# Kernel optimization log

Measured on AMD Instinct MI355X. Metric: run time of the kernel, lower is better.

Reference implementation:

```python
import jax, jax.numpy as jnp
import numpy as np

T, B, D, H, F, E = 2048, 2, 1024, 16, 4096, 8
HD = D // H
EPS = 1.1920929e-07  # torch.finfo(float32).eps


def setup_inputs() -> dict:
    key = jax.random.key(0)
    ks = jax.random.split(key, 20)
    sc = D ** -0.5
    n = lambda k, shape, s: jax.random.normal(k, shape, jnp.float32) * s
    return {
        "x": jax.random.normal(ks[0], (T, B, D), jnp.float32),
        "Wq": n(ks[1], (D, D), sc), "bq": jnp.zeros((D,), jnp.float32),
        "Wk": n(ks[2], (D, D), sc), "bk": jnp.zeros((D,), jnp.float32),
        "Wv": n(ks[3], (D, D), sc), "bv": jnp.zeros((D,), jnp.float32),
        "Wo": n(ks[4], (D, D), sc), "bo": jnp.zeros((D,), jnp.float32),
        "ln1_g": jnp.ones((D,), jnp.float32), "ln1_b": jnp.zeros((D,), jnp.float32),
        "ln2_g": jnp.ones((D,), jnp.float32), "ln2_b": jnp.zeros((D,), jnp.float32),
        "wg": n(ks[5], (D, E), sc),
        "W1": n(ks[6], (E, D, F), sc), "b1": jnp.zeros((E, F), jnp.float32),
        "W2": n(ks[7], (E, F, D), F ** -0.5), "b2": jnp.zeros((E, D), jnp.float32),
    }


def layer_norm(x, g, b):
    m = jnp.mean(x, -1, keepdims=True)
    v = jnp.var(x, -1, keepdims=True)
    return (x - m) * jax.lax.rsqrt(v + 1e-5) * g + b


def attention(x, Wq, bq, Wk, bk, Wv, bv, Wo, bo):
    t, b, d = x.shape
    q = ((x @ Wq + bq) * (HD ** -0.5)).reshape(t, b, H, HD)
    k = (x @ Wk + bk).reshape(t, b, H, HD)
    v = (x @ Wv + bv).reshape(t, b, H, HD)
    a = jax.nn.softmax(jnp.einsum('tbhd,sbhd->bhts', q, k), axis=-1)
    o = jnp.einsum('bhts,sbhd->tbhd', a, v).reshape(t, b, d)
    return o @ Wo + bo


def moe(xf, wg, W1, b1, W2, b2):
    # xf: [S, D] tokens (batch-major order, matching x.transpose(0,1).reshape(-1,d))
    S = xf.shape[0]
    C = 2 * ((S + E - 1) // E)  # fairseq top2 train capacity
    logits = xf.astype(jnp.float32) @ wg.astype(jnp.float32)
    gates = jax.nn.softmax(logits, axis=-1)
    idx1 = jnp.argmax(gates, axis=-1)
    m1 = jax.nn.one_hot(idx1, E, dtype=jnp.int32)
    idx2 = jnp.argmax(jnp.where(m1 > 0, -jnp.inf, logits), axis=-1)
    m2 = jax.nn.one_hot(idx2, E, dtype=jnp.int32)
    g1 = jnp.take_along_axis(gates, idx1[:, None], 1)[:, 0]
    g2 = jnp.take_along_axis(gates, idx2[:, None], 1)[:, 0]
    loc1 = jnp.cumsum(m1, axis=0) - 1
    loc2 = jnp.cumsum(m2, axis=0) - 1 + jnp.sum(m1, axis=0, keepdims=True)
    pos1 = jnp.sum(loc1 * m1, axis=1)
    pos2 = jnp.sum(loc2 * m2, axis=1)
    l_aux = jnp.mean(jnp.mean(gates, 0) * jnp.mean(m1.astype(jnp.float32), 0)) * E * E
    k1 = (pos1 < C).astype(xf.dtype)
    k2 = (pos2 < C).astype(xf.dtype)
    g1 = g1.astype(xf.dtype) * k1
    g2 = g2.astype(xf.dtype) * k2
    den = jnp.maximum(g1 + g2, EPS)
    g1, g2 = g1 / den, g2 / den
    f1 = idx1 * C + jnp.minimum(pos1, C - 1)
    f2 = idx2 * C + jnp.minimum(pos2, C - 1)
    # dispatch (unweighted, capacity-masked)
    buf = jnp.zeros((E * C, D), xf.dtype)
    buf = buf.at[f1].add(xf * k1[:, None]).at[f2].add(xf * k2[:, None])
    h = jax.nn.relu(jnp.einsum('ecd,edf->ecf', buf.reshape(E, C, D), W1) + b1[:, None, :])
    out = (jnp.einsum('ecf,efd->ecd', h, W2) + b2[:, None, :]).reshape(E * C, D)
    # combine with normalized gates (dropped tokens have zero gate)
    y = g1[:, None] * out[f1] + g2[:, None] * out[f2]
    return y, l_aux


def reference(x, Wq, bq, Wk, bk, Wv, bv, Wo, bo, ln1_g, ln1_b, ln2_g, ln2_b, wg, W1, b1, W2, b2):
    # pre-LN self-attention block
    residual = x
    h = layer_norm(x, ln1_g, ln1_b)
    h = attention(h, Wq, bq, Wk, bk, Wv, bv, Wo, bo)
    x = residual + h
    # pre-LN MoE FFN block
    residual = x
    h = layer_norm(x, ln2_g, ln2_b)
    hb = jnp.swapaxes(h, 0, 1).reshape(-1, D)  # [B*T, D]
    y, l_aux = moe(hb, wg, W1, b1, W2, b2)
    y = jnp.swapaxes(y.reshape(B, T, D), 0, 1)
    x = residual + y
    return x, l_aux
```

## Files before the change

kernel.cpp:

```cpp
#include <hip/hip_runtime.h>

#define TT 2048
#define BB 2
#define DD 1024
#define HH 16
#define HD 64
#define FF 4096
#define EE 8
#define SS (TT*BB)
#define CAP 1024
#define EPSF 1.1920929e-07f

typedef __attribute__((ext_vector_type(8))) short short8;
typedef __attribute__((ext_vector_type(4))) float floatx4;

static __device__ inline unsigned short f2bf(float f){
    unsigned int u = __float_as_uint(f);
    unsigned int r = (u + 0x7fffu + ((u>>16)&1u)) >> 16;
    return (unsigned short)r;
}
static __device__ inline float bf2f(unsigned short h){
    return __uint_as_float(((unsigned int)h)<<16);
}
static __device__ inline void split2(float x, unsigned short& h, unsigned short& l){
    unsigned short hh = f2bf(x);
    h = hh;
    l = f2bf(x - bf2f(hh));
}
#define GETF4(v,j) ((j)==0?(v).x:(j)==1?(v).y:(j)==2?(v).z:(v).w)

__global__ __launch_bounds__(256) void ln_kernel(const float* __restrict__ x,
    const float* __restrict__ gam, const float* __restrict__ bet, float* __restrict__ o)
{
    int row = blockIdx.x;
    int tid = threadIdx.x;
    float4 v = ((const float4*)(x + (size_t)row*DD))[tid];
    float s  = v.x+v.y+v.z+v.w;
    float ss = v.x*v.x+v.y*v.y+v.z*v.z+v.w*v.w;
    __shared__ float r1[256], r2[256];
    r1[tid]=s; r2[tid]=ss;
    __syncthreads();
    for (int off=128; off>0; off>>=1){
        if (tid<off){ r1[tid]+=r1[tid+off]; r2[tid]+=r2[tid+off]; }
        __syncthreads();
    }
    float mean = r1[0] * (1.f/DD);
    float var  = r2[0] * (1.f/DD) - mean*mean;
    float inv  = 1.f / sqrtf(var + 1e-5f);
    float4 g = ((const float4*)gam)[tid];
    float4 b = ((const float4*)bet)[tid];
    float4 r;
    r.x = (v.x-mean)*inv*g.x + b.x;
    r.y = (v.y-mean)*inv*g.y + b.y;
    r.z = (v.z-mean)*inv*g.z + b.z;
    r.w = (v.w-mean)*inv*g.w + b.w;
    ((float4*)(o + (size_t)row*DD))[tid] = r;
}

__global__ __launch_bounds__(256) void ln_split_kernel(const float* __restrict__ x,
    const float* __restrict__ gam, const float* __restrict__ bet,
    unsigned short* __restrict__ oh, unsigned short* __restrict__ ol)
{
    int row = blockIdx.x;
    int tid = threadIdx.x;
    float4 v = ((const float4*)(x + (size_t)row*DD))[tid];
    float s  = v.x+v.y+v.z+v.w;
    float ss = v.x*v.x+v.y*v.y+v.z*v.z+v.w*v.w;
    __shared__ float r1[256], r2[256];
    r1[tid]=s; r2[tid]=ss;
    __syncthreads();
    for (int off=128; off>0; off>>=1){
        if (tid<off){ r1[tid]+=r1[tid+off]; r2[tid]+=r2[tid+off]; }
        __syncthreads();
    }
    float mean = r1[0] * (1.f/DD);
    float var  = r2[0] * (1.f/DD) - mean*mean;
    float inv  = 1.f / sqrtf(var + 1e-5f);
    float4 g = ((const float4*)gam)[tid];
    float4 b = ((const float4*)bet)[tid];
    float4 r;
    r.x = (v.x-mean)*inv*g.x + b.x;
    r.y = (v.y-mean)*inv*g.y + b.y;
    r.z = (v.z-mean)*inv*g.z + b.z;
    r.w = (v.w-mean)*inv*g.w + b.w;
    ushort4 hv, lv;
    split2(r.x, hv.x, lv.x);
    split2(r.y, hv.y, lv.y);
    split2(r.z, hv.z, lv.z);
    split2(r.w, hv.w, lv.w);
    ((ushort4*)(oh + (size_t)row*DD))[tid] = hv;
    ((ushort4*)(ol + (size_t)row*DD))[tid] = lv;
}

template<bool RELU, bool OUTBF16>
__global__ __launch_bounds__(256) void gemm_mfma(
    const unsigned short* __restrict__ A, const unsigned short* __restrict__ Bt,
    const float* __restrict__ bias, float* __restrict__ Cf,
    unsigned short* __restrict__ Cb,
    int M, int N, int K, long wStride, int bStride, int rowsPerExp)
{
    __shared__ unsigned short As[128*64];
    __shared__ unsigned short Bs[128*64];
    const int tid = threadIdx.x, lane = tid&63;
    const int w = tid>>6, wr = w>>1, wc = w&1;
    int gx = gridDim.x;
    int nwg = gx*gridDim.y;
    int flat = blockIdx.y*gx + blockIdx.x;
    int qq = nwg>>3;
    flat = (flat&7)*qq + (flat>>3);
    const int m0 = (flat/gx)*128, n0 = (flat%gx)*128;
    const int e = m0 / rowsPerExp;
    const unsigned short* Bp = Bt + (size_t)e*wStride;
    const int srow = tid>>3, sslot = tid&7;
    floatx4 zf = {0.f,0.f,0.f,0.f};
    floatx4 acc[4][4];
    #pragma unroll
    for (int m=0;m<4;m++)
        #pragma unroll
        for (int n=0;n<4;n++) acc[m][n]=zf;

    short8 ar[4], br[4];
    #pragma unroll
    for (int i=0;i<4;i++){
        int r = srow + i*32;
        ar[i] = *(const short8*)(A  + (size_t)(m0+r)*K + sslot*8);
        br[i] = *(const short8*)(Bp + (size_t)(n0+r)*K + sslot*8);
    }
    const int NT = K/64;
    for (int kt=0; kt<NT; kt++){
        __syncthreads();
        #pragma unroll
        for (int i=0;i<4;i++){
            int r = srow + i*32;
            int off = r*64 + ((sslot ^ (r&7))<<3);
            *(short8*)(&As[off]) = ar[i];
            *(short8*)(&Bs[off]) = br[i];
        }
        __syncthreads();
        if (kt+1 < NT){
            int k0 = (kt+1)*64;
            #pragma unroll
            for (int i=0;i<4;i++){
                int r = srow + i*32;
                ar[i] = *(const short8*)(A  + (size_t)(m0+r)*K + k0 + sslot*8);
                br[i] = *(const short8*)(Bp + (size_t)(n0+r)*K + k0 + sslot*8);
            }
        }
        #pragma unroll
        for (int kk=0;kk<2;kk++){
            short8 af[4], bf[4];
            int kgrp = kk*4 + (lane>>4);
            #pragma unroll
            for (int m=0;m<4;m++){
                int rowa = wr*64 + m*16 + (lane&15);
                af[m] = *(const short8*)(&As[rowa*64 + ((kgrp ^ (rowa&7))<<3)]);
                int rowb = wc*64 + m*16 + (lane&15);
                bf[m] = *(const short8*)(&Bs[rowb*64 + ((kgrp ^ (rowb&7))<<3)]);
            }
            #pragma unroll
            for (int m=0;m<4;m++)
                #pragma unroll
                for (int n=0;n<4;n++)
                    acc[m][n] = __builtin_amdgcn_mfma_f32_16x16x32_bf16(af[m], bf[n], acc[m][n], 0,0,0);
        }
    }
    int colg = n0 + wc*64 + (lane&15);
    int rowg = m0 + wr*64 + ((lane>>4)<<2);
    #pragma unroll
    for (int n=0;n<4;n++){
        float bv = bias[e*bStride + colg + n*16];
        #pragma unroll
        for (int m=0;m<4;m++){
            #pragma unroll
            for (int i2=0;i2<4;i2++){
                float v = acc[m][n][i2] + bv;
                if (RELU) v = fmaxf(v, 0.f);
                size_t o = (size_t)(rowg + m*16 + i2)*N + colg + n*16;
                if (OUTBF16) Cb[o] = f2bf(v); else Cf[o] = v;
            }
        }
    }
}

template<bool QKV>
__global__ __launch_bounds__(256) void gemm_mfma_s(
    const unsigned short* __restrict__ Ahi, const unsigned short* __restrict__ Alo,
    const unsigned short* __restrict__ Bhi, const unsigned short* __restrict__ Blo,
    const float* __restrict__ b0, const float* __restrict__ b1p, const float* __restrict__ b2p,
    const float* __restrict__ res,
    float* __restrict__ o0,
    unsigned short* __restrict__ kh, unsigned short* __restrict__ kl,
    unsigned short* __restrict__ vh,
    int M, int K)
{
    __shared__ unsigned short As[128*64];
    __shared__ unsigned short Bs[128*64];
    const int tid = threadIdx.x, lane = tid&63;
    const int w = tid>>6, wr = w>>1, wc = w&1;
    const int m0 = blockIdx.y*128, n0 = blockIdx.x*128;
    const int row = tid>>1, khalf = tid&1;
    floatx4 zf = {0.f,0.f,0.f,0.f};
    floatx4 acc[4][4];
    #pragma unroll
    for (int m=0;m<4;m++)
        #pragma unroll
        for (int n=0;n<4;n++) acc[m][n]=zf;

    short8 awh0,awh1,awl0,awl1, bwh0,bwh1,bwl0,bwl1;
    {
        size_t ao = (size_t)(m0+row)*K + khalf*16;
        awh0 = *(const short8*)(Ahi+ao); awh1 = *(const short8*)(Ahi+ao+8);
        awl0 = *(const short8*)(Alo+ao); awl1 = *(const short8*)(Alo+ao+8);
        size_t bo = (size_t)(n0+row)*K + khalf*16;
        bwh0 = *(const short8*)(Bhi+bo); bwh1 = *(const short8*)(Bhi+bo+8);
        bwl0 = *(const short8*)(Blo+bo); bwl1 = *(const short8*)(Blo+bo+8);
    }
    const int NT = K/32;
    for (int kt=0; kt<NT; kt++){
        __syncthreads();
        {
            int base = row*64, sw = row&7;
            int g0 = khalf*2, g1 = khalf*2+1;
            *(short8*)(&As[base + ((g0^sw)<<3)])     = awh0;
            *(short8*)(&As[base + ((g1^sw)<<3)])     = awh1;
            *(short8*)(&As[base + (((g0+4)^sw)<<3)]) = awl0;
            *(short8*)(&As[base + (((g1+4)^sw)<<3)]) = awl1;
            *(short8*)(&Bs[base + ((g0^sw)<<3)])     = bwh0;
            *(short8*)(&Bs[base + ((g1^sw)<<3)])     = bwh1;
            *(short8*)(&Bs[base + (((g0+4)^sw)<<3)]) = bwl0;
            *(short8*)(&Bs[base + (((g1+4)^sw)<<3)]) = bwl1;
        }
        __syncthreads();
        if (kt+1 < NT){
            int k0 = (kt+1)*32;
            size_t ao = (size_t)(m0+row)*K + k0 + khalf*16;
            awh0 = *(const short8*)(Ahi+ao); awh1 = *(const short8*)(Ahi+ao+8);
            awl0 = *(const short8*)(Alo+ao); awl1 = *(const short8*)(Alo+ao+8);
            size_t bo = (size_t)(n0+row)*K + k0 + khalf*16;
            bwh0 = *(const short8*)(Bhi+bo); bwh1 = *(const short8*)(Bhi+bo+8);
            bwl0 = *(const short8*)(Blo+bo); bwl1 = *(const short8*)(Blo+bo+8);
        }
        {
            int kg = lane>>4;
            short8 afh[4], afl[4], bfh[4], bfl[4];
            #pragma unroll
            for (int m=0;m<4;m++){
                int ra = wr*64 + m*16 + (lane&15);
                afh[m] = *(const short8*)(&As[ra*64 + ((kg ^ (ra&7))<<3)]);
                afl[m] = *(const short8*)(&As[ra*64 + (((kg+4) ^ (ra&7))<<3)]);
                int rb = wc*64 + m*16 + (lane&15);
                bfh[m] = *(const short8*)(&Bs[rb*64 + ((kg ^ (rb&7))<<3)]);
                bfl[m] = *(const short8*)(&Bs[rb*64 + (((kg+4) ^ (rb&7))<<3)]);
            }
            #pragma unroll
            for (int m=0;m<4;m++)
                #pragma unroll
                for (int n=0;n<4;n++){
                    acc[m][n] = __builtin_amdgcn_mfma_f32_16x16x32_bf16(afl[m], bfh[n], acc[m][n], 0,0,0);
                    acc[m][n] = __builtin_amdgcn_mfma_f32_16x16x32_bf16(afh[m], bfl[n], acc[m][n], 0,0,0);
                    acc[m][n] = __builtin_amdgcn_mfma_f32_16x16x32_bf16(afh[m], bfh[n], acc[m][n], 0,0,0);
                }
        }
    }
    int colg = n0 + wc*64 + (lane&15);
    int rowg = m0 + wr*64 + ((lane>>4)<<2);
    if (QKV){
        int chunk = n0>>10;
        int colc = colg & 1023;
        const float* bp = chunk==0 ? b0 : (chunk==1 ? b1p : b2p);
        #pragma unroll
        for (int n=0;n<4;n++){
            float bv = bp[colc + n*16];
            #pragma unroll
            for (int m=0;m<4;m++){
                #pragma unroll
                for (int i2=0;i2<4;i2++){
                    int r = rowg + m*16 + i2;
                    float v = acc[m][n][i2] + bv;
                    size_t off = (size_t)r*DD + colc + n*16;
                    if (chunk==0){
                        o0[off] = v*0.125f;
                    } else if (chunk==1){
                        unsigned short hh, ll;
                        split2(v, hh, ll);
                        kh[off]=hh; kl[off]=ll;
                    } else {
                        vh[off] = f2bf(v);
                    }
                }
            }
        }
    } else {
        #pragma unroll
        for (int n=0;n<4;n++){
            float bv = b0[colg + n*16];
            #pragma unroll
            for (int m=0;m<4;m++){
                #pragma unroll
                for (int i2=0;i2<4;i2++){
                    int r = rowg + m*16 + i2;
                    float v = acc[m][n][i2] + bv + res[(size_t)r*DD + colg + n*16];
                    o0[(size_t)r*DD + colg + n*16] = v;
                }
            }
        }
    }
}

__global__ __launch_bounds__(512) void attn_mfma(const float* __restrict__ q,
    const unsigned short* __restrict__ khi, const unsigned short* __restrict__ klo,
    const unsigned short* __restrict__ vbf,
    unsigned short* __restrict__ ohi, unsigned short* __restrict__ olo)
{
    __shared__ unsigned short Kh[128*64], Kl[128*64];
    __shared__ unsigned short Vb[64*128];
    __shared__ unsigned short Ph[8*16*64];
    const int tid = threadIdx.x, lane = tid&63, w = tid>>6;
    const int t0 = blockIdx.x*128;
    const int b = blockIdx.y>>4, h = blockIdx.y&15;

    short8 qh[2], ql[2];
    #pragma unroll
    for (int kk=0;kk<2;kk++){
        const float* qp = q + ((size_t)(t0 + 16*w + (lane&15))*BB + b)*DD + h*64 + kk*32 + (lane>>4)*8;
        float4 f0 = ((const float4*)qp)[0];
        float4 f1 = ((const float4*)qp)[1];
        unsigned short hh[8], ll[8];
        #pragma unroll
        for (int j=0;j<4;j++){ split2(GETF4(f0,j), hh[j], ll[j]); }
        #pragma unroll
        for (int j=0;j<4;j++){ split2(GETF4(f1,j), hh[4+j], ll[4+j]); }
        qh[kk] = *(short8*)hh; ql[kk] = *(short8*)ll;
    }

    const int kr = tid>>2, kq = tid&3;
    const int vs0 = (tid&63)*2, vd0 = (tid>>6)*8;
    short8 kwh0,kwh1,kwl0,kwl1, vw0,vw1;
    {
        size_t ko = ((size_t)kr*BB + b)*DD + h*64 + kq*16;
        kwh0 = *(const short8*)(khi+ko); kwh1 = *(const short8*)(khi+ko+8);
        kwl0 = *(const short8*)(klo+ko); kwl1 = *(const short8*)(klo+ko+8);
        size_t vo = ((size_t)vs0*BB + b)*DD + h*64 + vd0;
        vw0 = *(const short8*)(vbf+vo);
        vw1 = *(const short8*)(vbf+vo + (size_t)BB*DD);
    }

    float m_st[4] = {-3.0e38f,-3.0e38f,-3.0e38f,-3.0e38f};
    float l_st[4] = {0.f,0.f,0.f,0.f};
    floatx4 zf = {0.f,0.f,0.f,0.f};
    floatx4 oacc[4];
    #pragma unroll
    for (int n=0;n<4;n++) oacc[n]=zf;

    for (int s0=0; s0<TT; s0+=128){
        __syncthreads();
        {
            int base = kr*64, sw = kr&7;
            int g0 = kq*2, g1 = kq*2+1;
            *(short8*)(&Kh[base + ((g0^sw)<<3)]) = kwh0;
            *(short8*)(&Kh[base + ((g1^sw)<<3)]) = kwh1;
            *(short8*)(&Kl[base + ((g0^sw)<<3)]) = kwl0;
            *(short8*)(&Kl[base + ((g1^sw)<<3)]) = kwl1;
        }
        {
            int g = vs0>>3, so = vs0&7;
            #pragma unroll
            for (int j=0;j<8;j++){
                int d = vd0 + j;
                ushort2 pv;
                pv.x = (unsigned short)vw0[j];
                pv.y = (unsigned short)vw1[j];
                *(ushort2*)(&Vb[d*128 + ((g ^ (d&7))<<3) + so]) = pv;
            }
        }
        __syncthreads();
        if (s0+128 < TT){
            size_t ko = ((size_t)(s0+128+kr)*BB + b)*DD + h*64 + kq*16;
            kwh0 = *(const short8*)(khi+ko); kwh1 = *(const short8*)(khi+ko+8);
            kwl0 = *(const short8*)(klo+ko); kwl1 = *(const short8*)(klo+ko+8);
            size_t vo = ((size_t)(s0+128+vs0)*BB + b)*DD + h*64 + vd0;
            vw0 = *(const short8*)(vbf+vo);
            vw1 = *(const short8*)(vbf+vo + (size_t)BB*DD);
        }
        floatx4 sacc[8];
        __builtin_amdgcn_s_setprio(1);
        #pragma unroll
        for (int n=0;n<8;n++){
            floatx4 s = zf;
            #pragma unroll
            for (int kk=0;kk<2;kk++){
                int g = kk*4 + (lane>>4);
                int rb = n*16 + (lane&15);
                short8 kbh = *(const short8*)(&Kh[rb*64 + ((g ^ (rb&7))<<3)]);
                short8 kbl = *(const short8*)(&Kl[rb*64 + ((g ^ (rb&7))<<3)]);
                s = __builtin_amdgcn_mfma_f32_16x16x32_bf16(ql[kk], kbh, s, 0,0,0);
                s = __builtin_amdgcn_mfma_f32_16x16x32_bf16(qh[kk], kbl, s, 0,0,0);
                s = __builtin_amdgcn_mfma_f32_16x16x32_bf16(qh[kk], kbh, s, 0,0,0);
            }
            sacc[n] = s;
        }
        __builtin_amdgcn_s_setprio(0);
        float mx[4];
        #pragma unroll
        for (int r=0;r<4;r++){
            float a0 = fmaxf(fmaxf(sacc[0][r], sacc[1][r]), fmaxf(sacc[2][r], sacc[3][r]));
            float a1 = fmaxf(fmaxf(sacc[4][r], sacc[5][r]), fmaxf(sacc[6][r], sacc[7][r]));
            mx[r] = fmaxf(a0, a1);
        }
        #pragma unroll
        for (int sh=1; sh<16; sh<<=1){
            #pragma unroll
            for (int r=0;r<4;r++) mx[r] = fmaxf(mx[r], __shfl_xor(mx[r], sh));
        }
        float corr[4];
        #pragma unroll
        for (int r=0;r<4;r++){
            float nm = fmaxf(m_st[r], mx[r]);
            corr[r] = __expf(m_st[r] - nm);
            m_st[r] = nm;
        }
        float ts[4] = {0.f,0.f,0.f,0.f};
        #pragma unroll
        for (int n=0;n<8;n++){
            #pragma unroll
            for (int r=0;r<4;r++){
                float p = __expf(sacc[n][r] - m_st[r]);
                ts[r] += p;
                sacc[n][r] = p;
            }
        }
        #pragma unroll
        for (int sh=1; sh<16; sh<<=1){
            #pragma unroll
            for (int r=0;r<4;r++) ts[r] += __shfl_xor(ts[r], sh);
        }
        #pragma unroll
        for (int r=0;r<4;r++) l_st[r] = l_st[r]*corr[r] + ts[r];
        #pragma unroll
        for (int n=0;n<4;n++)
            #pragma unroll
            for (int r=0;r<4;r++) oacc[n][r] *= corr[r];
        #pragma unroll
        for (int half=0; half<2; half++){
            #pragma unroll
            for (int n2=0;n2<4;n2++){
                int n = half*4 + n2;
                #pragma unroll
                for (int r=0;r<4;r++){
                    int q2 = ((lane>>4)<<2) + r;
                    int s2 = n2*16 + (lane&15);
                    int off = w*1024 + q2*64 + (((s2>>3) ^ (q2&7))<<3) + (s2&7);
                    Ph[off] = f2bf(sacc[n][r]);
                }
            }
            __builtin_amdgcn_s_setprio(1);
            #pragma unroll
            for (int kk=0;kk<2;kk++){
                int g = kk*4 + (lane>>4);
                int rq = lane&15;
                short8 pa = *(const short8*)(&Ph[w*1024 + rq*64 + ((g ^ (rq&7))<<3)]);
                #pragma unroll
                for (int n=0;n<4;n++){
                    int rd = n*16 + (lane&15);
                    int gv = half*8 + g;
                    short8 vb = *(const short8*)(&Vb[rd*128 + ((gv ^ (rd&7))<<3)]);
                    oacc[n] = __builtin_amdgcn_mfma_f32_16x16x32_bf16(pa, vb, oacc[n], 0,0,0);
                }
            }
            __builtin_amdgcn_s_setprio(0);
        }
    }
    float il[4];
    #pragma unroll
    for (int r=0;r<4;r++) il[r] = 1.f/l_st[r];
    int qrow = t0 + 16*w + ((lane>>4)<<2);
    #pragma unroll
    for (int n=0;n<4;n++){
        #pragma unroll
        for (int r=0;r<4;r++){
            float v = oacc[n][r]*il[r];
            unsigned short hh, ll;
            split2(v, hh, ll);
            size_t off = ((size_t)(qrow+r)*BB + b)*DD + h*64 + n*16 + (lane&15);
            ohi[off] = hh; olo[off] = ll;
        }
    }
}

__global__ __launch_bounds__(256) void transpose_bf16_k(const float* __restrict__ in,
    unsigned short* __restrict__ outp, int R, int C)
{
    __shared__ float t[64][65];
    int e = blockIdx.z;
    const float* ip = in + (size_t)e*R*C;
    unsigned short* op = outp + (size_t)e*R*C;
    int r0 = blockIdx.y*64, c0 = blockIdx.x*64;
    int tid = threadIdx.x;
    #pragma unroll
    for (int i=0;i<4;i++){
        int ch = i*256 + tid;
        int r = ch>>4, c4 = (ch&15)*4;
        float4 v = *(const float4*)(ip + (size_t)(r0+r)*C + c0 + c4);
        t[r][c4+0]=v.x; t[r][c4+1]=v.y; t[r][c4+2]=v.z; t[r][c4+3]=v.w;
    }
    __syncthreads();
    #pragma unroll
    for (int i=0;i<4;i++){
        int ch = i*256 + tid;
        int rr = ch>>4, c4 = (ch&15)*4;
        ushort4 o;
        o.x = f2bf(t[c4+0][rr]); o.y = f2bf(t[c4+1][rr]);
        o.z = f2bf(t[c4+2][rr]); o.w = f2bf(t[c4+3][rr]);
        *(ushort4*)(op + (size_t)(c0+rr)*R + r0 + c4) = o;
    }
}

__global__ __launch_bounds__(256) void transpose_split_k(const float* __restrict__ in,
    unsigned short* __restrict__ oh, unsigned short* __restrict__ ol, int R, int C)
{
    __shared__ float t[64][65];
    int r0 = blockIdx.y*64, c0 = blockIdx.x*64;
    int tid = threadIdx.x;
    #pragma unroll
    for (int i=0;i<4;i++){
        int ch = i*256 + tid;
        int r = ch>>4, c4 = (ch&15)*4;
        float4 v = *(const float4*)(in + (size_t)(r0+r)*C + c0 + c4);
        t[r][c4+0]=v.x; t[r][c4+1]=v.y; t[r][c4+2]=v.z; t[r][c4+3]=v.w;
    }
    __syncthreads();
    #pragma unroll
    for (int i=0;i<4;i++){
        int ch = i*256 + tid;
        int rr = ch>>4, c4 = (ch&15)*4;
        ushort4 hv, lv;
        split2(t[c4+0][rr], hv.x, lv.x);
        split2(t[c4+1][rr], hv.y, lv.y);
        split2(t[c4+2][rr], hv.z, lv.z);
        split2(t[c4+3][rr], hv.w, lv.w);
        size_t off = (size_t)(c0+rr)*R + r0 + c4;
        *(ushort4*)(oh + off) = hv;
        *(ushort4*)(ol + off) = lv;
    }
}

__global__ __launch_bounds__(256) void gather_bf16_k(const float* __restrict__ h2,
    const int* __restrict__ s2r, unsigned short* __restrict__ buf)
{
    int s = blockIdx.x; int row = s2r[s]; int c = threadIdx.x;
    float4 v = make_float4(0.f,0.f,0.f,0.f);
    if (row>=0) v = *(const float4*)(h2 + (size_t)row*DD + c*4);
    ushort4 o;
    o.x=f2bf(v.x); o.y=f2bf(v.y); o.z=f2bf(v.z); o.w=f2bf(v.w);
    *(ushort4*)(buf + (size_t)s*DD + c*4) = o;
}

__global__ __launch_bounds__(256) void route_kernel(const float* __restrict__ h2,
    const float* __restrict__ wgm, float* __restrict__ gates,
    int* __restrict__ idx1, int* __restrict__ idx2,
    float* __restrict__ g1, float* __restrict__ g2)
{
    int wid = threadIdx.x >> 6, lane = threadIdx.x & 63;
    int s = blockIdx.x*4 + wid;
    int row = (s % TT)*BB + (s / TT);
    const float* hr = h2 + (size_t)row*DD;
    float acc[EE] = {};
    #pragma unroll
    for (int c=0;c<16;c++){
        int d = c*64 + lane;
        float xv = hr[d];
        const float* wr = wgm + (size_t)d*EE;
        #pragma unroll
        for (int e2=0;e2<EE;e2++) acc[e2] += xv * wr[e2];
    }
    #pragma unroll
    for (int off=32; off>0; off>>=1){
        #pragma unroll
        for (int e2=0;e2<EE;e2++) acc[e2] += __shfl_down(acc[e2], off);
    }
    if (lane==0){
        float mx = acc[0];
        #pragma unroll
        for (int e2=1;e2<EE;e2++) mx = fmaxf(mx, acc[e2]);
        float ex[EE]; float sum=0.f;
        #pragma unroll
        for (int e2=0;e2<EE;e2++){ ex[e2] = __expf(acc[e2]-mx); sum += ex[e2]; }
        float inv = 1.f/sum;
        int i1=0; float bv1=acc[0];
        #pragma unroll
        for (int e2=1;e2<EE;e2++){ if (acc[e2] > bv1){ bv1=acc[e2]; i1=e2; } }
        int i2=-1; float bv2=-3.0e38f;
        #pragma unroll
        for (int e2=0;e2<EE;e2++){ if (e2!=i1 && acc[e2] > bv2){ bv2=acc[e2]; i2=e2; } }
        #pragma unroll
        for (int e2=0;e2<EE;e2++) gates[(size_t)s*EE + e2] = ex[e2]*inv;
        idx1[s]=i1; idx2[s]=i2;
        g1[s]=ex[i1]*inv; g2[s]=ex[i2]*inv;
    }
}

__global__ __launch_bounds__(256) void scan_kernel(
    const float* __restrict__ gates, const int* __restrict__ idx1, const int* __restrict__ idx2,
    const float* __restrict__ g1, const float* __restrict__ g2,
    float* __restrict__ g1n, float* __restrict__ g2n,
    int* __restrict__ f1, int* __restrict__ f2, int* __restrict__ slot2row,
    float* __restrict__ laux)
{
    __shared__ int i1s[SS];
    __shared__ int i2s[SS];
    __shared__ int cnt1[256][EE];
    __shared__ int cnt2[256][EE];
    __shared__ float gsum[256][EE];
    __shared__ int tot1[EE];
    int tid = threadIdx.x;
    for (int i=tid;i<EE*CAP;i+=256) slot2row[i] = -1;
    for (int i=tid;i<SS;i+=256){ i1s[i]=idx1[i]; i2s[i]=idx2[i]; }
    __syncthreads();
    int c1l[EE]={}, c2l[EE]={};
    float gl[EE]={};
    int base = tid*16;
    for (int qq=0;qq<16;qq++){
        int s = base+qq;
        c1l[i1s[s]]++; c2l[i2s[s]]++;
        #pragma unroll
        for (int e2=0;e2<EE;e2++) gl[e2] += gates[(size_t)s*EE+e2];
    }
    #pragma unroll
    for (int e2=0;e2<EE;e2++){ cnt1[tid][e2]=c1l[e2]; cnt2[tid][e2]=c2l[e2]; gsum[tid][e2]=gl[e2]; }
    __syncthreads();
    if (tid < EE){
        int e2 = tid;
        int run=0;
        for (int t=0;t<256;t++){ int tmp=cnt1[t][e2]; cnt1[t][e2]=run; run+=tmp; }
        tot1[e2]=run;
        run=0;
        for (int t=0;t<256;t++){ int tmp=cnt2[t][e2]; cnt2[t][e2]=run; run+=tmp; }
        float gr=0.f;
        for (int t=0;t<256;t++) gr += gsum[t][e2];
        gsum[0][e2]=gr;
    }
    __syncthreads();
    int p1[EE], p2[EE];
    #pragma unroll
    for (int e2=0;e2<EE;e2++){ p1[e2]=cnt1[tid][e2]; p2[e2]=cnt2[tid][e2]+tot1[e2]; }
    for (int qq=0;qq<16;qq++){
        int s = base+qq;
        int e1 = i1s[s], e2v = i2s[s];
        int pos1 = p1[e1]++;
        int pos2 = p2[e2v]++;
        float gv1 = g1[s], gv2 = g2[s];
        float gm1 = (pos1<CAP)? gv1 : 0.f;
        float gm2 = (pos2<CAP)? gv2 : 0.f;
        float den = fmaxf(gm1+gm2, EPSF);
        g1n[s] = gm1/den; g2n[s] = gm2/den;
        int ff1 = e1*CAP + (pos1<CAP?pos1:CAP-1);
        int ff2 = e2v*CAP + (pos2<CAP?pos2:CAP-1);
        f1[s]=ff1; f2[s]=ff2;
        int hrow = (s % TT)*BB + (s / TT);
        if (pos1<CAP) slot2row[ff1]=hrow;
        if (pos2<CAP) slot2row[ff2]=hrow;
    }
    if (tid==0){
        float a=0.f;
        #pragma unroll
        for (int e2=0;e2<EE;e2++) a += (gsum[0][e2]*(1.f/SS)) * ((float)tot1[e2]*(1.f/SS));
        laux[0] = a * (float)EE;
    }
}

__global__ __launch_bounds__(256) void combine_kernel(const float* __restrict__ x2,
    const float* __restrict__ eout, const float* __restrict__ g1n, const float* __restrict__ g2n,
    const int* __restrict__ f1, const int* __restrict__ f2, float* __restrict__ out)
{
    int s = blockIdx.x;
    float a = g1n[s], b = g2n[s];
    int s1 = f1[s], s2 = f2[s];
    int row = (s % TT)*BB + (s / TT);
    int c = threadIdx.x;
    float4 o1 = ((const float4*)(eout + (size_t)s1*DD))[c];
    float4 o2 = ((const float4*)(eout + (size_t)s2*DD))[c];
    float4 xr = ((const float4*)(x2 + (size_t)row*DD))[c];
    float4 r;
    r.x = xr.x + a*o1.x + b*o2.x;
    r.y = xr.y + a*o1.y + b*o2.y;
    r.z = xr.z + a*o1.z + b*o2.z;
    r.w = xr.w + a*o1.w + b*o2.w;
    ((float4*)(out + (size_t)row*DD))[c] = r;
}

extern "C" void kernel_launch(void* const* d_in, const int* in_sizes, int n_in,
                              void* d_out, int out_size, void* d_ws, size_t ws_size,
                              hipStream_t stream)
{
    const float* x    = (const float*)d_in[0];
    const float* Wq   = (const float*)d_in[1];
    const float* bq   = (const float*)d_in[2];
    const float* Wk   = (const float*)d_in[3];
    const float* bk   = (const float*)d_in[4];
    const float* Wv   = (const float*)d_in[5];
    const float* bv   = (const float*)d_in[6];
    const float* Wo   = (const float*)d_in[7];
    const float* bo   = (const float*)d_in[8];
    const float* ln1g = (const float*)d_in[9];
    const float* ln1b = (const float*)d_in[10];
    const float* ln2g = (const float*)d_in[11];
    const float* ln2b = (const float*)d_in[12];
    const float* wgm  = (const float*)d_in[13];
    const float* W1   = (const float*)d_in[14];
    const float* b1   = (const float*)d_in[15];
    const float* W2   = (const float*)d_in[16];
    const float* b2   = (const float*)d_in[17];
    float* out = (float*)d_out;

    char* w = (char*)d_ws;
    unsigned short* h1hi = (unsigned short*)(w);
    unsigned short* h1lo = (unsigned short*)(w + ((size_t)8<<20));
    float*          qb   = (float*)(w + ((size_t)16<<20));
    unsigned short* Khg  = (unsigned short*)(w + ((size_t)32<<20));
    unsigned short* Klg  = (unsigned short*)(w + ((size_t)40<<20));
    unsigned short* Vhg  = (unsigned short*)(w + ((size_t)48<<20));
    float*          x2   = (float*)(w + ((size_t)64<<20));
    unsigned short* bufb = (unsigned short*)(w + ((size_t)80<<20));
    unsigned short* hb   = (unsigned short*)(w + ((size_t)96<<20));
    unsigned short* Bqkv_hi = (unsigned short*)(w + ((size_t)96<<20));
    unsigned short* Bqkv_lo = (unsigned short*)(w + ((size_t)102<<20));
    unsigned short* Bo_hi   = (unsigned short*)(w + ((size_t)108<<20));
    unsigned short* Bo_lo   = (unsigned short*)(w + ((size_t)110<<20));
    unsigned short* W1t  = (unsigned short*)(w + ((size_t)160<<20));
    unsigned short* W2t  = (unsigned short*)(w + ((size_t)224<<20));
    float*          ffno = (float*)(w + ((size_t)32<<20));
    char*  sm   = w + ((size_t)288<<20);
    float* gates   = (float*)(sm);                sm += (size_t)SS*EE*4;
    int*   idx1    = (int*)(sm);                  sm += SS*4;
    int*   idx2    = (int*)(sm);                  sm += SS*4;
    float* g1      = (float*)(sm);                sm += SS*4;
    float* g2      = (float*)(sm);                sm += SS*4;
    float* g1n     = (float*)(sm);                sm += SS*4;
    float* g2n     = (float*)(sm);                sm += SS*4;
    int*   f1      = (int*)(sm);                  sm += SS*4;
    int*   f2      = (int*)(sm);                  sm += SS*4;
    int*   slot2row= (int*)(sm);                  sm += EE*CAP*4;

    transpose_bf16_k<<<dim3(FF/64, DD/64, EE), 256, 0, stream>>>(W1, W1t, DD, FF);
    transpose_bf16_k<<<dim3(DD/64, FF/64, EE), 256, 0, stream>>>(W2, W2t, FF, DD);
    transpose_split_k<<<dim3(16,16), 256, 0, stream>>>(Wq, Bqkv_hi,                   Bqkv_lo,                   DD, DD);
    transpose_split_k<<<dim3(16,16), 256, 0, stream>>>(Wk, Bqkv_hi + (size_t)DD*DD,   Bqkv_lo + (size_t)DD*DD,   DD, DD);
    transpose_split_k<<<dim3(16,16), 256, 0, stream>>>(Wv, Bqkv_hi + (size_t)2*DD*DD, Bqkv_lo + (size_t)2*DD*DD, DD, DD);
    transpose_split_k<<<dim3(16,16), 256, 0, stream>>>(Wo, Bo_hi, Bo_lo, DD, DD);
    ln_split_kernel<<<SS, 256, 0, stream>>>(x, ln1g, ln1b, h1hi, h1lo);
    gemm_mfma_s<true><<<dim3(24, SS/128), 256, 0, stream>>>(
        h1hi, h1lo, Bqkv_hi, Bqkv_lo, bq, bk, bv, nullptr, qb, Khg, Klg, Vhg, SS, DD);
    attn_mfma<<<dim3(TT/128, BB*HH), 512, 0, stream>>>(qb, Khg, Klg, Vhg, h1hi, h1lo);
    gemm_mfma_s<false><<<dim3(8, SS/128), 256, 0, stream>>>(
        h1hi, h1lo, Bo_hi, Bo_lo, bo, bo, bo, x, x2, nullptr, nullptr, nullptr, SS, DD);
    ln_kernel<<<SS, 256, 0, stream>>>(x2, ln2g, ln2b, qb);
    route_kernel<<<SS/4, 256, 0, stream>>>(qb, wgm, gates, idx1, idx2, g1, g2);
    scan_kernel<<<1, 256, 0, stream>>>(gates, idx1, idx2, g1, g2,
        g1n, g2n, f1, f2, slot2row, out + (size_t)SS*DD);
    gather_bf16_k<<<EE*CAP, 256, 0, stream>>>(qb, slot2row, bufb);
    gemm_mfma<true,true><<<dim3(FF/128, (EE*CAP)/128), 256, 0, stream>>>(
        bufb, W1t, b1, nullptr, hb, EE*CAP, FF, DD, (long)FF*DD, FF, CAP);
    gemm_mfma<false,false><<<dim3(DD/128, (EE*CAP)/128), 256, 0, stream>>>(
        hb, W2t, b2, ffno, nullptr, EE*CAP, DD, FF, (long)DD*FF, DD, CAP);
    combine_kernel<<<SS, 256, 0, stream>>>(x2, ffno, g1n, g2n, f1, f2, out);
    (void)in_sizes; (void)n_in; (void)out_size; (void)ws_size;
}
```

Before: 616.6 us.

## Double-buffer LDS tiles in MFMA GEMMs to drop one barrier per k-step

Both GEMM kernels now keep two shared-memory tile buffers. Each iteration computes from the current buffer, then writes the prefetched next tile into the other buffer and syncs once, so there is one barrier per k-iteration instead of two. This is meant to cut synchronisation stalls and let LDS writes overlap with other waves' compute. In exchange LDS use doubles to 64KB per block, which may lower occupancy.

```diff
diff --git a/kernel.cpp b/kernel.cpp
--- a/kernel.cpp
+++ b/kernel.cpp
@@ -99,8 +99,8 @@
     unsigned short* __restrict__ Cb,
     int M, int N, int K, long wStride, int bStride, int rowsPerExp)
 {
-    __shared__ unsigned short As[128*64];
-    __shared__ unsigned short Bs[128*64];
+    __shared__ unsigned short As[2][128*64];
+    __shared__ unsigned short Bs[2][128*64];
     const int tid = threadIdx.x, lane = tid&63;
     const int w = tid>>6, wr = w>>1, wc = w&1;
     int gx = gridDim.x;
@@ -126,17 +126,17 @@
         ar[i] = *(const short8*)(A  + (size_t)(m0+r)*K + sslot*8);
         br[i] = *(const short8*)(Bp + (size_t)(n0+r)*K + sslot*8);
     }
+    #pragma unroll
+    for (int i=0;i<4;i++){
+        int r = srow + i*32;
+        int off = r*64 + ((sslot ^ (r&7))<<3);
+        *(short8*)(&As[0][off]) = ar[i];
+        *(short8*)(&Bs[0][off]) = br[i];
+    }
+    __syncthreads();
     const int NT = K/64;
+    int cur = 0;
     for (int kt=0; kt<NT; kt++){
-        __syncthreads();
-        #pragma unroll
-        for (int i=0;i<4;i++){
-            int r = srow + i*32;
-            int off = r*64 + ((sslot ^ (r&7))<<3);
-            *(short8*)(&As[off]) = ar[i];
-            *(short8*)(&Bs[off]) = br[i];
-        }
-        __syncthreads();
         if (kt+1 < NT){
             int k0 = (kt+1)*64;
             #pragma unroll
@@ -153,15 +153,27 @@
             #pragma unroll
             for (int m=0;m<4;m++){
                 int rowa = wr*64 + m*16 + (lane&15);
-                af[m] = *(const short8*)(&As[rowa*64 + ((kgrp ^ (rowa&7))<<3)]);
+                af[m] = *(const short8*)(&As[cur][rowa*64 + ((kgrp ^ (rowa&7))<<3)]);
                 int rowb = wc*64 + m*16 + (lane&15);
-                bf[m] = *(const short8*)(&Bs[rowb*64 + ((kgrp ^ (rowb&7))<<3)]);
+                bf[m] = *(const short8*)(&Bs[cur][rowb*64 + ((kgrp ^ (rowb&7))<<3)]);
             }
             #pragma unroll
             for (int m=0;m<4;m++)
                 #pragma unroll
                 for (int n=0;n<4;n++)
                     acc[m][n] = __builtin_amdgcn_mfma_f32_16x16x32_bf16(af[m], bf[n], acc[m][n], 0,0,0);
+        }
+        if (kt+1 < NT){
+            int nb = cur^1;
+            #pragma unroll
+            for (int i=0;i<4;i++){
+                int r = srow + i*32;
+                int off = r*64 + ((sslot ^ (r&7))<<3);
+                *(short8*)(&As[nb][off]) = ar[i];
+                *(short8*)(&Bs[nb][off]) = br[i];
+            }
+            __syncthreads();
+            cur = nb;
         }
     }
     int colg = n0 + wc*64 + (lane&15);
@@ -193,8 +205,8 @@
     unsigned short* __restrict__ vh,
     int M, int K)
 {
-    __shared__ unsigned short As[128*64];
-    __shared__ unsigned short Bs[128*64];
+    __shared__ unsigned short As[2][128*64];
+    __shared__ unsigned short Bs[2][128*64];
     const int tid = threadIdx.x, lane = tid&63;
     const int w = tid>>6, wr = w>>1, wc = w&1;
     const int m0 = blockIdx.y*128, n0 = blockIdx.x*128;
@@ -215,22 +227,22 @@
         bwh0 = *(const short8*)(Bhi+bo); bwh1 = *(const short8*)(Bhi+bo+8);
         bwl0 = *(const short8*)(Blo+bo); bwl1 = *(const short8*)(Blo+bo+8);
     }
+    {
+        int base = row*64, sw = row&7;
+        int g0 = khalf*2, g1 = khalf*2+1;
+        *(short8*)(&As[0][base + ((g0^sw)<<3)])     = awh0;
+        *(short8*)(&As[0][base + ((g1^sw)<<3)])     = awh1;
+        *(short8*)(&As[0][base + (((g0+4)^sw)<<3)]) = awl0;
+        *(short8*)(&As[0][base + (((g1+4)^sw)<<3)]) = awl1;
+        *(short8*)(&Bs[0][base + ((g0^sw)<<3)])     = bwh0;
+        *(short8*)(&Bs[0][base + ((g1^sw)<<3)])     = bwh1;
+        *(short8*)(&Bs[0][base + (((g0+4)^sw)<<3)]) = bwl0;
+        *(short8*)(&Bs[0][base + (((g1+4)^sw)<<3)]) = bwl1;
+    }
+    __syncthreads();
     const int NT = K/32;
+    int cur = 0;
     for (int kt=0; kt<NT; kt++){
-        __syncthreads();
-        {
-            int base = row*64, sw = row&7;
-            int g0 = khalf*2, g1 = khalf*2+1;
-            *(short8*)(&As[base + ((g0^sw)<<3)])     = awh0;
-            *(short8*)(&As[base + ((g1^sw)<<3)])     = awh1;
-            *(short8*)(&As[base + (((g0+4)^sw)<<3)]) = awl0;
-            *(short8*)(&As[base + (((g1+4)^sw)<<3)]) = awl1;
-            *(short8*)(&Bs[base + ((g0^sw)<<3)])     = bwh0;
-            *(short8*)(&Bs[base + ((g1^sw)<<3)])     = bwh1;
-            *(short8*)(&Bs[base + (((g0+4)^sw)<<3)]) = bwl0;
-            *(short8*)(&Bs[base + (((g1+4)^sw)<<3)]) = bwl1;
-        }
-        __syncthreads();
         if (kt+1 < NT){
             int k0 = (kt+1)*32;
             size_t ao = (size_t)(m0+row)*K + k0 + khalf*16;
@@ -246,11 +258,11 @@
             #pragma unroll
             for (int m=0;m<4;m++){
                 int ra = wr*64 + m*16 + (lane&15);
-                afh[m] = *(const short8*)(&As[ra*64 + ((kg ^ (ra&7))<<3)]);
-                afl[m] = *(const short8*)(&As[ra*64 + (((kg+4) ^ (ra&7))<<3)]);
+                afh[m] = *(const short8*)(&As[cur][ra*64 + ((kg ^ (ra&7))<<3)]);
+                afl[m] = *(const short8*)(&As[cur][ra*64 + (((kg+4) ^ (ra&7))<<3)]);
                 int rb = wc*64 + m*16 + (lane&15);
-                bfh[m] = *(const short8*)(&Bs[rb*64 + ((kg ^ (rb&7))<<3)]);
-                bfl[m] = *(const short8*)(&Bs[rb*64 + (((kg+4) ^ (rb&7))<<3)]);
+                bfh[m] = *(const short8*)(&Bs[cur][rb*64 + ((kg ^ (rb&7))<<3)]);
+                bfl[m] = *(const short8*)(&Bs[cur][rb*64 + (((kg+4) ^ (rb&7))<<3)]);
             }
             #pragma unroll
             for (int m=0;m<4;m++)
@@ -260,6 +272,21 @@
                     acc[m][n] = __builtin_amdgcn_mfma_f32_16x16x32_bf16(afh[m], bfl[n], acc[m][n], 0,0,0);
                     acc[m][n] = __builtin_amdgcn_mfma_f32_16x16x32_bf16(afh[m], bfh[n], acc[m][n], 0,0,0);
                 }
+        }
+        if (kt+1 < NT){
+            int nb = cur^1;
+            int base = row*64, sw = row&7;
+            int g0 = khalf*2, g1 = khalf*2+1;
+            *(short8*)(&As[nb][base + ((g0^sw)<<3)])     = awh0;
+            *(short8*)(&As[nb][base + ((g1^sw)<<3)])     = awh1;
+            *(short8*)(&As[nb][base + (((g0+4)^sw)<<3)]) = awl0;
+            *(short8*)(&As[nb][base + (((g1+4)^sw)<<3)]) = awl1;
+            *(short8*)(&Bs[nb][base + ((g0^sw)<<3)])     = bwh0;
+            *(short8*)(&Bs[nb][base + ((g1^sw)<<3)])     = bwh1;
+            *(short8*)(&Bs[nb][base + (((g0+4)^sw)<<3)]) = bwl0;
+            *(short8*)(&Bs[nb][base + (((g1+4)^sw)<<3)]) = bwl1;
+            __syncthreads();
+            cur = nb;
         }
     }
     int colg = n0 + wc*64 + (lane&15);
```

After: 618.4 us. About the same (+0.3%).
